# Optimization experiments

Hardware: AMD Instinct MI355X
Metric: run time of the kernel (lower is better)

The kernel has to match this reference:

```python
import jax, jax.numpy as jnp
import numpy as np

KEY_SIZE = 256

def setup_inputs() -> dict:
    key = jax.random.key(0)
    ks = jax.random.split(key, 4)
    B, C, T, K, V = 4, 512, 4096, 256, 256
    s = 1.0 / np.sqrt(C)
    return {
        "x": jax.random.normal(ks[0], (B, C, T), dtype=jnp.float32),
        "Wq": jax.random.normal(ks[1], (C, K), dtype=jnp.float32) * s,
        "bq": jnp.zeros((K,), dtype=jnp.float32),
        "Wk": jax.random.normal(ks[2], (C, K), dtype=jnp.float32) * s,
        "bk": jnp.zeros((K,), dtype=jnp.float32),
        "Wv": jax.random.normal(ks[3], (C, V), dtype=jnp.float32) * s,
        "bv": jnp.zeros((V,), dtype=jnp.float32),
    }

def reference(x, Wq, bq, Wk, bk, Wv, bv):
    # x: (B, C, T) -> (B, T, C)
    B, C, T = x.shape
    x_bt = jnp.transpose(x, (0, 2, 1))
    q = x_bt @ Wq + bq            # (B, T, K)
    k = x_bt @ Wk + bk            # (B, T, K)
    v = x_bt @ Wv + bv            # (B, T, V)
    logits = jnp.einsum('btk,bsk->bts', q, k) / jnp.sqrt(jnp.float32(KEY_SIZE))
    causal = jnp.tril(jnp.ones((T, T), dtype=bool))  # keep lower-triangular incl diag
    logits = jnp.where(causal, logits, -jnp.inf)
    attn = jax.nn.softmax(logits, axis=-1)
    read = jnp.einsum('bts,bsv->btv', attn, v)        # (B, T, V)
    out = jnp.concatenate([x_bt, read], axis=-1)      # (B, T, C+V)
    return jnp.transpose(out, (0, 2, 1))              # (B, C+V, T)
```

## Files before the change

### kernel.cpp

```cpp
#include <hip/hip_runtime.h>
#include <stdint.h>

#define Bn 4
#define Cn 512
#define Tn 4096
#define Kn 256
#define Nall 768

typedef __attribute__((ext_vector_type(8))) short bf16x8;
typedef __attribute__((ext_vector_type(4))) float f32x4;

__device__ __forceinline__ unsigned short f2bf(float f) {
  union { float f; unsigned int u; } v; v.f = f;
  unsigned int r = v.u + 0x7fffu + ((v.u >> 16) & 1u);
  return (unsigned short)(r >> 16);
}

__device__ __forceinline__ void gload_lds16(const void* g, void* l) {
  auto gp = reinterpret_cast<const __attribute__((address_space(1))) unsigned int*>(
      reinterpret_cast<uintptr_t>(g));
  auto lp = reinterpret_cast<__attribute__((address_space(3))) unsigned int*>(
      static_cast<unsigned int>(reinterpret_cast<uintptr_t>(l)));
  __builtin_amdgcn_global_load_lds(gp, lp, 16, 0, 0);
}

__device__ __forceinline__ f32x4 mfma16(bf16x8 a, bf16x8 b, f32x4 c) {
  return __builtin_amdgcn_mfma_f32_16x16x32_bf16(a, b, c, 0, 0, 0);
}

__global__ __launch_bounds__(256) void prep_x_kernel(const float* __restrict__ x,
    float* __restrict__ out, unsigned short* __restrict__ xt) {
  const int tt = blockIdx.x, cc = blockIdx.y, b = blockIdx.z;
  __shared__ unsigned short tile[64][66];
  const int tid = threadIdx.x;
#pragma unroll
  for (int e = 0; e < 4; ++e) {
    int f = e * 256 + tid;
    int row = f >> 4, c4 = f & 15;
    size_t gi = ((size_t)(b * Cn + cc * 64 + row)) * Tn + tt * 64 + c4 * 4;
    float4 v = *(const float4*)(x + gi);
    size_t go = ((size_t)(b * Nall + cc * 64 + row)) * Tn + tt * 64 + c4 * 4;
    *(float4*)(out + go) = v;
    tile[row][c4 * 4 + 0] = f2bf(v.x);
    tile[row][c4 * 4 + 1] = f2bf(v.y);
    tile[row][c4 * 4 + 2] = f2bf(v.z);
    tile[row][c4 * 4 + 3] = f2bf(v.w);
  }
  __syncthreads();
#pragma unroll
  for (int e = 0; e < 2; ++e) {
    int f = e * 256 + tid;
    int trow = f >> 3, cv = f & 7;
    bf16x8 vv;
#pragma unroll
    for (int j = 0; j < 8; ++j) vv[j] = (short)tile[cv * 8 + j][trow];
    *(bf16x8*)(xt + ((size_t)(b * Tn) + tt * 64 + trow) * Cn + cc * 64 + cv * 8) = vv;
  }
}

__global__ __launch_bounds__(256) void prep_w_kernel(const float* __restrict__ Wq,
    const float* __restrict__ Wk, const float* __restrict__ Wv,
    const float* __restrict__ bq, const float* __restrict__ bk, const float* __restrict__ bv,
    unsigned short* __restrict__ wt, float* __restrict__ bias) {
  int idx = blockIdx.x * 256 + threadIdx.x;
  int n = idx >> 9, c = idx & 511;
  const float* W = (n < 256) ? Wq : ((n < 512) ? Wk : Wv);
  wt[idx] = f2bf(W[c * 256 + (n & 255)]);
  if (idx < Nall) {
    const float* bb = (idx < 256) ? bq : ((idx < 512) ? bk : bv);
    bias[idx] = bb[idx & 255];
  }
}

__global__ __launch_bounds__(256) void qkv_gemm_kernel(const unsigned short* __restrict__ xt,
    const unsigned short* __restrict__ wt, const float* __restrict__ bias,
    unsigned short* __restrict__ qb, unsigned short* __restrict__ kb,
    unsigned short* __restrict__ vt) {
  const int t0 = blockIdx.x * 128, n0 = blockIdx.y * 128, b = blockIdx.z;
  __shared__ char at[8192];
  __shared__ char bt[8192];
  const int tid = threadIdx.x, w = tid >> 6, lane = tid & 63, g = lane >> 4, lr = lane & 15;
  const int wm = w >> 1, wn = w & 1;
  f32x4 acc[4][4];
#pragma unroll
  for (int i = 0; i < 4; ++i)
#pragma unroll
    for (int j = 0; j < 4; ++j) acc[i][j] = (f32x4){0.f, 0.f, 0.f, 0.f};

  const unsigned short* xtp = xt + ((size_t)b * Tn + t0) * Cn;
  for (int c0 = 0; c0 < Cn; c0 += 32) {
    __syncthreads();
#pragma unroll
    for (int i = 0; i < 2; ++i) {
      int off = i * 4096 + w * 1024 + lane * 16;
      int row = off >> 6, col = off & 63;
      gload_lds16(xtp + (size_t)row * Cn + c0 + (col >> 1), at + i * 4096 + w * 1024);
      gload_lds16(wt + (size_t)(n0 + row) * Cn + c0 + (col >> 1), bt + i * 4096 + w * 1024);
    }
    __syncthreads();
    bf16x8 af[4], bfr[4];
#pragma unroll
    for (int mt = 0; mt < 4; ++mt)
      af[mt] = *(const bf16x8*)(at + (wm * 64 + mt * 16 + lr) * 64 + g * 16);
#pragma unroll
    for (int nt = 0; nt < 4; ++nt)
      bfr[nt] = *(const bf16x8*)(bt + (wn * 64 + nt * 16 + lr) * 64 + g * 16);
#pragma unroll
    for (int mt = 0; mt < 4; ++mt)
#pragma unroll
      for (int nt = 0; nt < 4; ++nt)
        acc[mt][nt] = mfma16(af[mt], bfr[nt], acc[mt][nt]);
  }
#pragma unroll
  for (int nt = 0; nt < 4; ++nt) {
    int n = n0 + wn * 64 + nt * 16 + lr;
    float bval = bias[n];
#pragma unroll
    for (int mt = 0; mt < 4; ++mt) {
#pragma unroll
      for (int r = 0; r < 4; ++r) {
        int t = t0 + wm * 64 + mt * 16 + g * 4 + r;
        unsigned short h = f2bf(acc[mt][nt][r] + bval);
        if (n < 256) {
          qb[((size_t)(b * Tn) + t) * Kn + n] = h;
        } else if (n < 512) {
          int nc = n - 256;
          kb[((size_t)(b * Tn) + t) * Kn + (nc ^ ((t & 7) << 3))] = h;
        } else {
          int vc = n - 512;
          int tl = t & 63;
          vt[((size_t)(b * Kn) + vc) * Tn + (t & ~63) + (tl ^ ((vc & 7) << 3))] = h;
        }
      }
    }
  }
}

#define STAGE(s_, par_) do {                                                   \
    const int s0_ = (s_) * 64;                                                 \
    char* kd_ = kbase + (par_) * 32768;                                        \
    char* vd_ = vbase + (par_) * 32768;                                        \
    _Pragma("unroll")                                                          \
    for (int i2 = 0; i2 < 4; ++i2) {                                           \
      int off_ = i2 * 8192 + tid * 16;                                         \
      int krow_ = off_ >> 9, kcol_ = off_ & 511;                               \
      gload_lds16(kbp + (size_t)(s0_ + krow_) * Kn + (kcol_ >> 1), kd_ + off_);\
      int vrow_ = off_ >> 7, vcol_ = off_ & 127;                               \
      gload_lds16(vtp + (size_t)vrow_ * Tn + s0_ + (vcol_ >> 1), vd_ + off_);  \
    }                                                                          \
  } while (0)

__global__ __launch_bounds__(512) void attn_kernel(const unsigned short* __restrict__ qb,
    const unsigned short* __restrict__ kb, const unsigned short* __restrict__ vt,
    float* __restrict__ po, float* __restrict__ ml, float* __restrict__ out) {
  const int wg = blockIdx.x;
  const int b = (wg >> 1) & 3;
  int item = ((wg >> 3) << 1) | (wg & 1);
  item = (item * 53) % 80;
  int t = 0, c = 0, preP = 0, accum = 0;
  for (t = 0; t < 32; ++t) {
    int cnt = (t + 8) >> 3;
    if (item < accum + cnt) { c = item - accum; break; }
    accum += cnt;
    if (t >= 8) preP += cnt;
  }
  const bool direct = (t < 8);
  const int slot = b * 72 + preP + c;
  const int qt0 = t << 7;
  const int sb = c * 16, se = min(sb + 16, 2 * t + 2);

  __shared__ char smem[147456];
  char* kbase = smem;
  char* vbase = smem + 65536;
  char* pbuf  = smem + 131072;
  const int tid = threadIdx.x, w = tid >> 6, lane = tid & 63, g = lane >> 4, lr = lane & 15;
  const float SCL = 0.09016844005555521f;

  const unsigned short* kbp = kb + (size_t)(b * Tn) * Kn;
  const unsigned short* vtp = vt + (size_t)(b * Kn) * Tn;

  const unsigned short* qrow = qb + ((size_t)(b * Tn) + qt0 + w * 16 + lr) * Kn;
  bf16x8 qf[8];
#pragma unroll
  for (int kc = 0; kc < 8; ++kc) qf[kc] = *(const bf16x8*)(qrow + kc * 32 + g * 8);

  f32x4 o[16];
#pragma unroll
  for (int nt = 0; nt < 16; ++nt) o[nt] = (f32x4){0.f, 0.f, 0.f, 0.f};
  float m2[4], lsum[4];
#pragma unroll
  for (int r = 0; r < 4; ++r) { m2[r] = -1e30f; lsum[r] = 0.f; }
  char* pbw = pbuf + w * 2048;

  STAGE(sb, 0);
  __syncthreads();
  int cur = 0;
  for (int s = sb; s < se; ++s) {
    const int s0 = s * 64;
    if (s + 1 < se) STAGE(s + 1, cur ^ 1);
    char* kcur = kbase + cur * 32768;
    char* vcur = vbase + cur * 32768;

    f32x4 sfr[4];
#pragma unroll
    for (int ct = 0; ct < 4; ++ct) sfr[ct] = (f32x4){0.f, 0.f, 0.f, 0.f};
#pragma unroll
    for (int kc = 0; kc < 8; ++kc) {
#pragma unroll
      for (int ct = 0; ct < 4; ++ct) {
        int srow = ct * 16 + lr;
        bf16x8 kf = *(const bf16x8*)(kcur + srow * 512 +
                                     ((kc * 64 + g * 16) ^ ((srow & 7) << 4)));
        sfr[ct] = mfma16(qf[kc], kf, sfr[ct]);
      }
    }

    float sv[4][4];
    const bool diag = (s0 >= qt0);
#pragma unroll
    for (int ct = 0; ct < 4; ++ct)
#pragma unroll
      for (int r = 0; r < 4; ++r) {
        float v = sfr[ct][r] * SCL;
        if (diag) {
          int trow = qt0 + w * 16 + g * 4 + r;
          int scol = s0 + ct * 16 + lr;
          if (scol > trow) v = -1e30f;
        }
        sv[ct][r] = v;
      }
    float mt_[4];
#pragma unroll
    for (int r = 0; r < 4; ++r)
      mt_[r] = fmaxf(fmaxf(sv[0][r], sv[1][r]), fmaxf(sv[2][r], sv[3][r]));
#pragma unroll
    for (int d = 1; d < 16; d <<= 1)
#pragma unroll
      for (int r = 0; r < 4; ++r)
        mt_[r] = fmaxf(mt_[r], __shfl_xor(mt_[r], d, 64));
    float al[4], rs[4];
#pragma unroll
    for (int r = 0; r < 4; ++r) {
      float mn = fmaxf(m2[r], mt_[r]);
      al[r] = __builtin_amdgcn_exp2f(m2[r] - mn);
      m2[r] = mn;
      rs[r] = 0.f;
    }
    unsigned short ph[4][4];
#pragma unroll
    for (int ct = 0; ct < 4; ++ct)
#pragma unroll
      for (int r = 0; r < 4; ++r) {
        float p = __builtin_amdgcn_exp2f(sv[ct][r] - m2[r]);
        rs[r] += p;
        ph[ct][r] = f2bf(p);
      }
#pragma unroll
    for (int d = 1; d < 16; d <<= 1)
#pragma unroll
      for (int r = 0; r < 4; ++r)
        rs[r] += __shfl_xor(rs[r], d, 64);
#pragma unroll
    for (int r = 0; r < 4; ++r) lsum[r] = lsum[r] * al[r] + rs[r];
#pragma unroll
    for (int nt = 0; nt < 16; ++nt)
#pragma unroll
      for (int r = 0; r < 4; ++r) o[nt][r] *= al[r];

#pragma unroll
    for (int ct = 0; ct < 4; ++ct)
#pragma unroll
      for (int r = 0; r < 4; ++r) {
        int row = g * 4 + r;
        int colb = (ct * 16 + lr) * 2;
        *(unsigned short*)(pbw + row * 128 + (colb ^ ((row & 7) << 4))) = ph[ct][r];
      }
    bf16x8 pa[2];
#pragma unroll
    for (int kc2 = 0; kc2 < 2; ++kc2)
      pa[kc2] = *(const bf16x8*)(pbw + lr * 128 +
                                 ((kc2 * 64 + g * 16) ^ ((lr & 7) << 4)));
#pragma unroll
    for (int nt = 0; nt < 16; ++nt) {
      int vrow = nt * 16 + lr;
#pragma unroll
      for (int kc2 = 0; kc2 < 2; ++kc2) {
        bf16x8 vf = *(const bf16x8*)(vcur + vrow * 128 +
                                     ((kc2 * 64 + g * 16) ^ ((vrow & 7) << 4)));
        o[nt] = mfma16(pa[kc2], vf, o[nt]);
      }
    }

    __syncthreads();
    cur ^= 1;
  }

  if (direct) {
    float inv[4];
#pragma unroll
    for (int r = 0; r < 4; ++r) inv[r] = 1.0f / lsum[r];
    float* outp = out + ((size_t)(b * Nall) + 512) * Tn;
#pragma unroll
    for (int nt = 0; nt < 16; ++nt)
#pragma unroll
      for (int r = 0; r < 4; ++r)
        outp[(size_t)(nt * 16 + lr) * Tn + qt0 + w * 16 + g * 4 + r] = o[nt][r] * inv[r];
  } else {
    float* pob = po + (size_t)slot * 32768;
#pragma unroll
    for (int nt = 0; nt < 16; ++nt)
#pragma unroll
      for (int r = 0; r < 4; ++r)
        pob[(w * 16 + g * 4 + r) * 256 + nt * 16 + lr] = o[nt][r];
    if (lr == 0) {
#pragma unroll
      for (int r = 0; r < 4; ++r) {
        ml[(size_t)slot * 256 + w * 16 + g * 4 + r] = m2[r];
        ml[(size_t)slot * 256 + 128 + w * 16 + g * 4 + r] = lsum[r];
      }
    }
  }
}

__global__ __launch_bounds__(256) void merge_kernel(const float* __restrict__ po,
    const float* __restrict__ ml, float* __restrict__ out) {
  const int tt = blockIdx.x + 8;
  const int b = blockIdx.y, zg = blockIdx.z;
  const int nc = (tt + 8) >> 3;
  int preP = 0;
  for (int u = 8; u < tt; ++u) preP += (u + 8) >> 3;
  const int slot0 = b * 72 + preP;
  const int tid = threadIdx.x;

  __shared__ float wrow[32][4];
  if (tid < 32) {
    int r = zg * 32 + tid;
    float M = -1e30f;
    for (int cc = 0; cc < nc; ++cc)
      M = fmaxf(M, ml[(size_t)(slot0 + cc) * 256 + r]);
    float e[4], L = 0.f;
    for (int cc = 0; cc < nc; ++cc) {
      e[cc] = __builtin_amdgcn_exp2f(ml[(size_t)(slot0 + cc) * 256 + r] - M);
      L += ml[(size_t)(slot0 + cc) * 256 + 128 + r] * e[cc];
    }
    float linv = 1.0f / L;
    for (int cc = 0; cc < nc; ++cc) wrow[tid][cc] = e[cc] * linv;
  }
  __syncthreads();

  const int n = tid;
  float* outp = out + ((size_t)(b * Nall + 512 + n)) * Tn + tt * 128 + zg * 32;
  for (int r4 = 0; r4 < 8; ++r4) {
    float4 vv;
#pragma unroll
    for (int j = 0; j < 4; ++j) {
      int rl = r4 * 4 + j;
      int rr = zg * 32 + rl;
      float val = 0.f;
      for (int cc = 0; cc < nc; ++cc)
        val += wrow[rl][cc] * po[(size_t)(slot0 + cc) * 32768 + rr * 256 + n];
      vv[j] = val;
    }
    *(float4*)(outp + r4 * 4) = vv;
  }
}

extern "C" void kernel_launch(void* const* d_in, const int* in_sizes, int n_in,
                              void* d_out, int out_size, void* d_ws, size_t ws_size,
                              hipStream_t stream) {
  const float* x  = (const float*)d_in[0];
  const float* Wq = (const float*)d_in[1];
  const float* bq = (const float*)d_in[2];
  const float* Wk = (const float*)d_in[3];
  const float* bk = (const float*)d_in[4];
  const float* Wv = (const float*)d_in[5];
  const float* bv = (const float*)d_in[6];
  float* out = (float*)d_out;
  char* ws = (char*)d_ws;

  unsigned short* qb = (unsigned short*)(ws);
  unsigned short* kb = (unsigned short*)(ws + 8388608);
  unsigned short* vt = (unsigned short*)(ws + 16777216);
  unsigned short* xt = (unsigned short*)(ws + 25165824);
  unsigned short* wt = (unsigned short*)(ws + 41943040);
  float*        bias = (float*)(ws + 42729472);
  float*          po = (float*)(ws + 25165824);
  float*          mlb = (float*)(ws + 62914560);

  prep_w_kernel<<<1536, 256, 0, stream>>>(Wq, Wk, Wv, bq, bk, bv, wt, bias);
  prep_x_kernel<<<dim3(64, 8, 4), 256, 0, stream>>>(x, out, xt);
  qkv_gemm_kernel<<<dim3(32, 6, 4), 256, 0, stream>>>(xt, wt, bias, qb, kb, vt);
  attn_kernel<<<320, 512, 0, stream>>>(qb, kb, vt, po, mlb, out);
  merge_kernel<<<dim3(24, 4, 4), 256, 0, stream>>>(po, mlb, out);
}
```

Baseline: 278.6 us.

## Restructure attention: 256-thread blocks, two row tiles per wave, finer KV split

The attention kernel now runs 256-thread blocks with two blocks per CU, and each wave handles 32 query rows (two 16-row tiles) so every K/V fragment read from LDS feeds two MFMAs. The KV split is finer (8 tiles per chunk, 576 blocks), and fully masked tiles are skipped per wave. Rescaling happens lazily, only when the running max grows by more than a threshold. Row sums are computed with an MFMA against a ones vector, and partial outputs are stored as bf16 to halve merge traffic. Double-buffered async staging is replaced by a single buffer with two barriers per tile, which removes load/compute overlap. The bf16 partials also add rounding error to the merged result.

```diff
diff --git a/kernel.cpp b/kernel.cpp
--- a/kernel.cpp
+++ b/kernel.cpp
@@ -14,6 +14,10 @@
   union { float f; unsigned int u; } v; v.f = f;
   unsigned int r = v.u + 0x7fffu + ((v.u >> 16) & 1u);
   return (unsigned short)(r >> 16);
+}
+
+__device__ __forceinline__ float bf2f(unsigned short h) {
+  union { unsigned int u; float f; } v; v.u = ((unsigned int)h) << 16; return v.f;
 }
 
 __device__ __forceinline__ void gload_lds16(const void* g, void* l) {
@@ -136,215 +140,238 @@
   }
 }
 
-#define STAGE(s_, par_) do {                                                   \
-    const int s0_ = (s_) * 64;                                                 \
-    char* kd_ = kbase + (par_) * 32768;                                        \
-    char* vd_ = vbase + (par_) * 32768;                                        \
-    _Pragma("unroll")                                                          \
-    for (int i2 = 0; i2 < 4; ++i2) {                                           \
-      int off_ = i2 * 8192 + tid * 16;                                         \
-      int krow_ = off_ >> 9, kcol_ = off_ & 511;                               \
-      gload_lds16(kbp + (size_t)(s0_ + krow_) * Kn + (kcol_ >> 1), kd_ + off_);\
-      int vrow_ = off_ >> 7, vcol_ = off_ & 127;                               \
-      gload_lds16(vtp + (size_t)vrow_ * Tn + s0_ + (vcol_ >> 1), vd_ + off_);  \
-    }                                                                          \
-  } while (0)
-
-__global__ __launch_bounds__(512) void attn_kernel(const unsigned short* __restrict__ qb,
+__global__ __launch_bounds__(256, 2) void attn_kernel(const unsigned short* __restrict__ qb,
     const unsigned short* __restrict__ kb, const unsigned short* __restrict__ vt,
-    float* __restrict__ po, float* __restrict__ ml, float* __restrict__ out) {
+    unsigned short* __restrict__ po, float* __restrict__ ml, float* __restrict__ out) {
   const int wg = blockIdx.x;
   const int b = (wg >> 1) & 3;
   int item = ((wg >> 3) << 1) | (wg & 1);
-  item = (item * 53) % 80;
+  item = (item * 59) % 144;
   int t = 0, c = 0, preP = 0, accum = 0;
   for (t = 0; t < 32; ++t) {
-    int cnt = (t + 8) >> 3;
+    int cnt = (t + 4) >> 2;
     if (item < accum + cnt) { c = item - accum; break; }
     accum += cnt;
-    if (t >= 8) preP += cnt;
-  }
-  const bool direct = (t < 8);
-  const int slot = b * 72 + preP + c;
+    if (t >= 4) preP += cnt;
+  }
+  const bool direct = (t < 4);
+  const int slot = b * 140 + preP + c;
   const int qt0 = t << 7;
-  const int sb = c * 16, se = min(sb + 16, 2 * t + 2);
-
-  __shared__ char smem[147456];
-  char* kbase = smem;
-  char* vbase = smem + 65536;
-  char* pbuf  = smem + 131072;
+  const int sb = c * 8, se = min(sb + 8, 2 * t + 2);
+
+  __shared__ char smem[81920];
+  char* kbuf = smem;
+  char* vbuf = smem + 32768;
+  char* pbuf = smem + 65536;
   const int tid = threadIdx.x, w = tid >> 6, lane = tid & 63, g = lane >> 4, lr = lane & 15;
   const float SCL = 0.09016844005555521f;
+  const int wrow0 = qt0 + w * 32;
 
   const unsigned short* kbp = kb + (size_t)(b * Tn) * Kn;
   const unsigned short* vtp = vt + (size_t)(b * Kn) * Tn;
 
-  const unsigned short* qrow = qb + ((size_t)(b * Tn) + qt0 + w * 16 + lr) * Kn;
-  bf16x8 qf[8];
-#pragma unroll
-  for (int kc = 0; kc < 8; ++kc) qf[kc] = *(const bf16x8*)(qrow + kc * 32 + g * 8);
-
-  f32x4 o[16];
-#pragma unroll
-  for (int nt = 0; nt < 16; ++nt) o[nt] = (f32x4){0.f, 0.f, 0.f, 0.f};
-  float m2[4], lsum[4];
-#pragma unroll
-  for (int r = 0; r < 4; ++r) { m2[r] = -1e30f; lsum[r] = 0.f; }
-  char* pbw = pbuf + w * 2048;
-
-  STAGE(sb, 0);
-  __syncthreads();
-  int cur = 0;
+  bf16x8 qf[2][8];
+#pragma unroll
+  for (int mt = 0; mt < 2; ++mt) {
+    const unsigned short* qrow = qb + ((size_t)(b * Tn) + wrow0 + mt * 16 + lr) * Kn;
+#pragma unroll
+    for (int kc = 0; kc < 8; ++kc) qf[mt][kc] = *(const bf16x8*)(qrow + kc * 32 + g * 8);
+  }
+
+  bf16x8 onef;
+#pragma unroll
+  for (int j = 0; j < 8; ++j) onef[j] = (short)0x3F80;
+
+  f32x4 o[2][16];
+#pragma unroll
+  for (int mt = 0; mt < 2; ++mt)
+#pragma unroll
+    for (int nt = 0; nt < 16; ++nt) o[mt][nt] = (f32x4){0.f, 0.f, 0.f, 0.f};
+  float m2[2][4], ls[2][4];
+#pragma unroll
+  for (int mt = 0; mt < 2; ++mt)
+#pragma unroll
+    for (int r = 0; r < 4; ++r) { m2[mt][r] = -1e30f; ls[mt][r] = 0.f; }
+  char* pbw = pbuf + w * 4096;
+
   for (int s = sb; s < se; ++s) {
     const int s0 = s * 64;
-    if (s + 1 < se) STAGE(s + 1, cur ^ 1);
-    char* kcur = kbase + cur * 32768;
-    char* vcur = vbase + cur * 32768;
-
-    f32x4 sfr[4];
-#pragma unroll
-    for (int ct = 0; ct < 4; ++ct) sfr[ct] = (f32x4){0.f, 0.f, 0.f, 0.f};
-#pragma unroll
-    for (int kc = 0; kc < 8; ++kc) {
-#pragma unroll
-      for (int ct = 0; ct < 4; ++ct) {
-        int srow = ct * 16 + lr;
-        bf16x8 kf = *(const bf16x8*)(kcur + srow * 512 +
-                                     ((kc * 64 + g * 16) ^ ((srow & 7) << 4)));
-        sfr[ct] = mfma16(qf[kc], kf, sfr[ct]);
+    __syncthreads();
+#pragma unroll
+    for (int i2 = 0; i2 < 8; ++i2) {
+      int off = i2 * 4096 + tid * 16;
+      { int row = off >> 9, col = off & 511;
+        gload_lds16(kbp + (size_t)(s0 + row) * Kn + (col >> 1), kbuf + off); }
+      { int row = off >> 7, col = off & 127;
+        gload_lds16(vtp + (size_t)row * Tn + s0 + (col >> 1), vbuf + off); }
+    }
+    __syncthreads();
+
+    if (s0 < wrow0 + 32) {
+      f32x4 sfr[2][4];
+#pragma unroll
+      for (int mt = 0; mt < 2; ++mt)
+#pragma unroll
+        for (int ct = 0; ct < 4; ++ct) sfr[mt][ct] = (f32x4){0.f, 0.f, 0.f, 0.f};
+#pragma unroll
+      for (int kc = 0; kc < 8; ++kc) {
+#pragma unroll
+        for (int ct = 0; ct < 4; ++ct) {
+          int srow = ct * 16 + lr;
+          bf16x8 kf = *(const bf16x8*)(kbuf + srow * 512 +
+                                       ((kc * 64 + g * 16) ^ ((srow & 7) << 4)));
+          sfr[0][ct] = mfma16(qf[0][kc], kf, sfr[0][ct]);
+          sfr[1][ct] = mfma16(qf[1][kc], kf, sfr[1][ct]);
+        }
       }
-    }
-
-    float sv[4][4];
-    const bool diag = (s0 >= qt0);
-#pragma unroll
-    for (int ct = 0; ct < 4; ++ct)
-#pragma unroll
-      for (int r = 0; r < 4; ++r) {
-        float v = sfr[ct][r] * SCL;
-        if (diag) {
-          int trow = qt0 + w * 16 + g * 4 + r;
-          int scol = s0 + ct * 16 + lr;
-          if (scol > trow) v = -1e30f;
+
+      const bool needmask = (s0 + 64 > wrow0);
+#pragma unroll
+      for (int mt = 0; mt < 2; ++mt) {
+        float sv[4][4];
+#pragma unroll
+        for (int ct = 0; ct < 4; ++ct)
+#pragma unroll
+          for (int r = 0; r < 4; ++r) {
+            float v = sfr[mt][ct][r] * SCL;
+            if (needmask) {
+              int trow = wrow0 + mt * 16 + g * 4 + r;
+              int scol = s0 + ct * 16 + lr;
+              if (scol > trow) v = -1e30f;
+            }
+            sv[ct][r] = v;
+          }
+        float mx[4];
+#pragma unroll
+        for (int r = 0; r < 4; ++r)
+          mx[r] = fmaxf(fmaxf(sv[0][r], sv[1][r]), fmaxf(sv[2][r], sv[3][r]));
+#pragma unroll
+        for (int d = 1; d < 16; d <<= 1)
+#pragma unroll
+          for (int r = 0; r < 4; ++r)
+            mx[r] = fmaxf(mx[r], __shfl_xor(mx[r], d, 64));
+        int stable = 1;
+#pragma unroll
+        for (int r = 0; r < 4; ++r) stable &= (mx[r] <= m2[mt][r] + 8.0f);
+        if (!__all(stable)) {
+#pragma unroll
+          for (int r = 0; r < 4; ++r) {
+            float mn = fmaxf(m2[mt][r], mx[r]);
+            float al = __builtin_amdgcn_exp2f(m2[mt][r] - mn);
+            m2[mt][r] = mn;
+            ls[mt][r] *= al;
+#pragma unroll
+            for (int nt = 0; nt < 16; ++nt) o[mt][nt][r] *= al;
+          }
         }
-        sv[ct][r] = v;
+        unsigned short ph[4][4];
+#pragma unroll
+        for (int ct = 0; ct < 4; ++ct)
+#pragma unroll
+          for (int r = 0; r < 4; ++r)
+            ph[ct][r] = f2bf(__builtin_amdgcn_exp2f(sv[ct][r] - m2[mt][r]));
+#pragma unroll
+        for (int ct = 0; ct < 4; ++ct)
+#pragma unroll
+          for (int r = 0; r < 4; ++r) {
+            int row = g * 4 + r;
+            int colb = (ct * 16 + lr) * 2;
+            *(unsigned short*)(pbw + mt * 2048 + row * 128 + (colb ^ ((row & 7) << 4))) = ph[ct][r];
+          }
       }
-    float mt_[4];
-#pragma unroll
-    for (int r = 0; r < 4; ++r)
-      mt_[r] = fmaxf(fmaxf(sv[0][r], sv[1][r]), fmaxf(sv[2][r], sv[3][r]));
-#pragma unroll
-    for (int d = 1; d < 16; d <<= 1)
-#pragma unroll
-      for (int r = 0; r < 4; ++r)
-        mt_[r] = fmaxf(mt_[r], __shfl_xor(mt_[r], d, 64));
-    float al[4], rs[4];
-#pragma unroll
-    for (int r = 0; r < 4; ++r) {
-      float mn = fmaxf(m2[r], mt_[r]);
-      al[r] = __builtin_amdgcn_exp2f(m2[r] - mn);
-      m2[r] = mn;
-      rs[r] = 0.f;
-    }
-    unsigned short ph[4][4];
-#pragma unroll
-    for (int ct = 0; ct < 4; ++ct)
-#pragma unroll
-      for (int r = 0; r < 4; ++r) {
-        float p = __builtin_amdgcn_exp2f(sv[ct][r] - m2[r]);
-        rs[r] += p;
-        ph[ct][r] = f2bf(p);
+
+      bf16x8 pa[2][2];
+#pragma unroll
+      for (int mt = 0; mt < 2; ++mt)
+#pragma unroll
+        for (int kc2 = 0; kc2 < 2; ++kc2)
+          pa[mt][kc2] = *(const bf16x8*)(pbw + mt * 2048 + lr * 128 +
+                                         ((kc2 * 64 + g * 16) ^ ((lr & 7) << 4)));
+      f32x4 lacc[2];
+      lacc[0] = (f32x4){0.f, 0.f, 0.f, 0.f};
+      lacc[1] = (f32x4){0.f, 0.f, 0.f, 0.f};
+#pragma unroll
+      for (int kc2 = 0; kc2 < 2; ++kc2) {
+        lacc[0] = mfma16(pa[0][kc2], onef, lacc[0]);
+        lacc[1] = mfma16(pa[1][kc2], onef, lacc[1]);
       }
 #pragma unroll
-    for (int d = 1; d < 16; d <<= 1)
-#pragma unroll
-      for (int r = 0; r < 4; ++r)
-        rs[r] += __shfl_xor(rs[r], d, 64);
-#pragma unroll
-    for (int r = 0; r < 4; ++r) lsum[r] = lsum[r] * al[r] + rs[r];
-#pragma unroll
-    for (int nt = 0; nt < 16; ++nt)
-#pragma unroll
-      for (int r = 0; r < 4; ++r) o[nt][r] *= al[r];
-
-#pragma unroll
-    for (int ct = 0; ct < 4; ++ct)
-#pragma unroll
-      for (int r = 0; r < 4; ++r) {
-        int row = g * 4 + r;
-        int colb = (ct * 16 + lr) * 2;
-        *(unsigned short*)(pbw + row * 128 + (colb ^ ((row & 7) << 4))) = ph[ct][r];
+      for (int nt = 0; nt < 16; ++nt) {
+        int vrow = nt * 16 + lr;
+#pragma unroll
+        for (int kc2 = 0; kc2 < 2; ++kc2) {
+          bf16x8 vf = *(const bf16x8*)(vbuf + vrow * 128 +
+                                       ((kc2 * 64 + g * 16) ^ ((vrow & 7) << 4)));
+          o[0][nt] = mfma16(pa[0][kc2], vf, o[0][nt]);
+          o[1][nt] = mfma16(pa[1][kc2], vf, o[1][nt]);
+        }
       }
-    bf16x8 pa[2];
-#pragma unroll
-    for (int kc2 = 0; kc2 < 2; ++kc2)
-      pa[kc2] = *(const bf16x8*)(pbw + lr * 128 +
-                                 ((kc2 * 64 + g * 16) ^ ((lr & 7) << 4)));
-#pragma unroll
-    for (int nt = 0; nt < 16; ++nt) {
-      int vrow = nt * 16 + lr;
-#pragma unroll
-      for (int kc2 = 0; kc2 < 2; ++kc2) {
-        bf16x8 vf = *(const bf16x8*)(vcur + vrow * 128 +
-                                     ((kc2 * 64 + g * 16) ^ ((vrow & 7) << 4)));
-        o[nt] = mfma16(pa[kc2], vf, o[nt]);
-      }
-    }
-
-    __syncthreads();
-    cur ^= 1;
+#pragma unroll
+      for (int mt = 0; mt < 2; ++mt)
+#pragma unroll
+        for (int r = 0; r < 4; ++r) ls[mt][r] += lacc[mt][r];
+    }
   }
 
   if (direct) {
-    float inv[4];
-#pragma unroll
-    for (int r = 0; r < 4; ++r) inv[r] = 1.0f / lsum[r];
     float* outp = out + ((size_t)(b * Nall) + 512) * Tn;
 #pragma unroll
-    for (int nt = 0; nt < 16; ++nt)
-#pragma unroll
-      for (int r = 0; r < 4; ++r)
-        outp[(size_t)(nt * 16 + lr) * Tn + qt0 + w * 16 + g * 4 + r] = o[nt][r] * inv[r];
+    for (int mt = 0; mt < 2; ++mt) {
+      float inv[4];
+#pragma unroll
+      for (int r = 0; r < 4; ++r) inv[r] = 1.0f / ls[mt][r];
+#pragma unroll
+      for (int nt = 0; nt < 16; ++nt)
+#pragma unroll
+        for (int r = 0; r < 4; ++r)
+          outp[(size_t)(nt * 16 + lr) * Tn + wrow0 + mt * 16 + g * 4 + r] = o[mt][nt][r] * inv[r];
+    }
   } else {
-    float* pob = po + (size_t)slot * 32768;
-#pragma unroll
-    for (int nt = 0; nt < 16; ++nt)
-#pragma unroll
-      for (int r = 0; r < 4; ++r)
-        pob[(w * 16 + g * 4 + r) * 256 + nt * 16 + lr] = o[nt][r];
+    unsigned short* pob = po + (size_t)slot * 32768;
+#pragma unroll
+    for (int mt = 0; mt < 2; ++mt)
+#pragma unroll
+      for (int nt = 0; nt < 16; ++nt)
+#pragma unroll
+        for (int r = 0; r < 4; ++r)
+          pob[(w * 32 + mt * 16 + g * 4 + r) * 256 + nt * 16 + lr] = f2bf(o[mt][nt][r]);
     if (lr == 0) {
 #pragma unroll
-      for (int r = 0; r < 4; ++r) {
-        ml[(size_t)slot * 256 + w * 16 + g * 4 + r] = m2[r];
-        ml[(size_t)slot * 256 + 128 + w * 16 + g * 4 + r] = lsum[r];
-      }
-    }
-  }
-}
-
-__global__ __launch_bounds__(256) void merge_kernel(const float* __restrict__ po,
+      for (int mt = 0; mt < 2; ++mt)
+#pragma unroll
+        for (int r = 0; r < 4; ++r) {
+          int row = w * 32 + mt * 16 + g * 4 + r;
+          ml[(size_t)slot * 256 + row] = m2[mt][r];
+          ml[(size_t)slot * 256 + 128 + row] = ls[mt][r];
+        }
+    }
+  }
+}
+
+__global__ __launch_bounds__(256) void merge_kernel(const unsigned short* __restrict__ po,
     const float* __restrict__ ml, float* __restrict__ out) {
-  const int tt = blockIdx.x + 8;
+  const int tt = blockIdx.x + 4;
   const int b = blockIdx.y, zg = blockIdx.z;
-  const int nc = (tt + 8) >> 3;
+  const int nc = (tt + 4) >> 2;
   int preP = 0;
-  for (int u = 8; u < tt; ++u) preP += (u + 8) >> 3;
-  const int slot0 = b * 72 + preP;
+  for (int u = 4; u < tt; ++u) preP += (u + 4) >> 2;
+  const int slot0 = b * 140 + preP;
   const int tid = threadIdx.x;
 
-  __shared__ float wrow[32][4];
+  __shared__ float wrow[32][8];
   if (tid < 32) {
     int r = zg * 32 + tid;
     float M = -1e30f;
     for (int cc = 0; cc < nc; ++cc)
       M = fmaxf(M, ml[(size_t)(slot0 + cc) * 256 + r]);
-    float e[4], L = 0.f;
+    float L = 0.f;
     for (int cc = 0; cc < nc; ++cc) {
-      e[cc] = __builtin_amdgcn_exp2f(ml[(size_t)(slot0 + cc) * 256 + r] - M);
-      L += ml[(size_t)(slot0 + cc) * 256 + 128 + r] * e[cc];
+      float e = __builtin_amdgcn_exp2f(ml[(size_t)(slot0 + cc) * 256 + r] - M);
+      wrow[tid][cc] = e;
+      L += ml[(size_t)(slot0 + cc) * 256 + 128 + r] * e;
     }
     float linv = 1.0f / L;
-    for (int cc = 0; cc < nc; ++cc) wrow[tid][cc] = e[cc] * linv;
+    for (int cc = 0; cc < nc; ++cc) wrow[tid][cc] *= linv;
   }
   __syncthreads();
 
@@ -358,7 +385,7 @@
       int rr = zg * 32 + rl;
       float val = 0.f;
       for (int cc = 0; cc < nc; ++cc)
-        val += wrow[rl][cc] * po[(size_t)(slot0 + cc) * 32768 + rr * 256 + n];
+        val += wrow[rl][cc] * bf2f(po[(size_t)(slot0 + cc) * 32768 + rr * 256 + n]);
       vv[j] = val;
     }
     *(float4*)(outp + r4 * 4) = vv;
@@ -384,12 +411,12 @@
   unsigned short* xt = (unsigned short*)(ws + 25165824);
   unsigned short* wt = (unsigned short*)(ws + 41943040);
   float*        bias = (float*)(ws + 42729472);
-  float*          po = (float*)(ws + 25165824);
-  float*          mlb = (float*)(ws + 62914560);
+  unsigned short* po = (unsigned short*)(ws + 25165824);
+  float*         mlb = (float*)(ws + 61865984);
 
   prep_w_kernel<<<1536, 256, 0, stream>>>(Wq, Wk, Wv, bq, bk, bv, wt, bias);
   prep_x_kernel<<<dim3(64, 8, 4), 256, 0, stream>>>(x, out, xt);
   qkv_gemm_kernel<<<dim3(32, 6, 4), 256, 0, stream>>>(xt, wt, bias, qb, kb, vt);
-  attn_kernel<<<320, 512, 0, stream>>>(qb, kb, vt, po, mlb, out);
-  merge_kernel<<<dim3(24, 4, 4), 256, 0, stream>>>(po, mlb, out);
-}
+  attn_kernel<<<576, 256, 0, stream>>>(qb, kb, vt, po, mlb, out);
+  merge_kernel<<<dim3(28, 4, 4), 256, 0, stream>>>(po, mlb, out);
+}
```

New measurement: 424.1 us. 52.2% more time.
